# Kernel tuning notes

Hardware: AMD Instinct MI355X
Metric: run time of the kernel (lower is better)

Reference implementation:

```python
import jax, jax.numpy as jnp
import numpy as np

H = 12
D_MODEL = 768
H_D = D_MODEL // H


def setup_inputs() -> dict:
    key = jax.random.key(0)
    ks = jax.random.split(key, 11)
    B, S = 2, 2048
    scale_in = 1.0
    w_scale = 1.0 / np.sqrt(D_MODEL)
    inp = {
        "query": jax.random.normal(ks[0], (B, S, D_MODEL), dtype=jnp.float32),
        "key": jax.random.normal(ks[1], (B, S, D_MODEL), dtype=jnp.float32),
        "value": jax.random.normal(ks[2], (B, S, D_MODEL), dtype=jnp.float32),
        "wq": jax.random.normal(ks[3], (D_MODEL, D_MODEL), dtype=jnp.float32) * w_scale,
        "bq": jnp.zeros((D_MODEL,), dtype=jnp.float32),
        "wk": jax.random.normal(ks[4], (D_MODEL, D_MODEL), dtype=jnp.float32) * w_scale,
        "bk": jnp.zeros((D_MODEL,), dtype=jnp.float32),
        "wv": jax.random.normal(ks[5], (D_MODEL, D_MODEL), dtype=jnp.float32) * w_scale,
        "bv": jnp.zeros((D_MODEL,), dtype=jnp.float32),
        "wo": jax.random.normal(ks[6], (D_MODEL, D_MODEL), dtype=jnp.float32) * w_scale,
        "bo": jnp.zeros((D_MODEL,), dtype=jnp.float32),
    }
    return inp


def reference(query, key, value, wq, bq, wk, bk, wv, bv, wo, bo):
    B, S, _ = query.shape
    # QKV projections, split into heads: [B, H, S, h_d]
    def proj(x, w, b):
        y = jnp.einsum("bsd,de->bse", x, w) + b
        return y.reshape(B, S, H, H_D).transpose(0, 2, 1, 3)

    q = proj(query, wq, bq)
    k = proj(key, wk, bk)
    v = proj(value, wv, bv)

    # scaled dot-product attention (dropout disabled / eval mode)
    scores = jnp.einsum("bhsd,bhtd->bhst", q, k) / jnp.sqrt(jnp.float32(H_D))
    wm = jax.nn.softmax(scores, axis=-1)  # [B, H, S, S]
    out = jnp.einsum("bhst,bhtd->bhsd", wm, v)

    # merge heads and output projection
    out = out.transpose(0, 2, 1, 3).reshape(B, S, D_MODEL)
    out = jnp.einsum("bsd,de->bse", out, wo) + bo
    return out
```

## Files before the change

### kernel.cpp

```cpp
#include <hip/hip_runtime.h>

#define H 12
#define DM 768
#define HD 64
#define SEQ 2048
#define BATCH 2
#define MROWS (BATCH*SEQ)

typedef __attribute__((ext_vector_type(8))) short short8;
typedef __attribute__((ext_vector_type(4))) float f32x4;
typedef __attribute__((ext_vector_type(16))) float f32x16;
using u16 = unsigned short;
using u32 = unsigned int;

__device__ __forceinline__ float bf2f(u16 u) { return __uint_as_float(((u32)u) << 16); }
__device__ __forceinline__ u16 f2bf(float x) {
  u32 u = __float_as_uint(x);
  return (u16)((u + 0x7fffu + ((u >> 16) & 1u)) >> 16);
}
__device__ __forceinline__ u32 cvt_pk_bf16(float lo, float hi) {
  u32 r;
  asm("v_cvt_pk_bf16_f32 %0, %1, %2" : "=v"(r) : "v"(lo), "v"(hi));
  return r;
}
__device__ __forceinline__ void gl2lds16(const u16* __restrict__ g, u16* l) {
  __builtin_amdgcn_global_load_lds(
      (const __attribute__((address_space(1))) unsigned int*)g,
      (__attribute__((address_space(3))) unsigned int*)l,
      16, 0, 0);
}

#define C_SM 0.18033688011112042f

__global__ __launch_bounds__(256) void transpose_w4(const float* __restrict__ w0, const float* __restrict__ w1,
                                                    const float* __restrict__ w2, const float* __restrict__ w3,
                                                    u16* __restrict__ dst0)
{
  __shared__ u16 Ts[64][72];
  const float* src = blockIdx.z == 0 ? w0 : blockIdx.z == 1 ? w1 : blockIdx.z == 2 ? w2 : w3;
  u16* dst = dst0 + (size_t)blockIdx.z * DM * DM;
  const int t = threadIdx.x;
  const int r0 = blockIdx.y * 64, c0 = blockIdx.x * 64;
  const int row = t >> 2, cq = (t & 3) * 16;
  const float* sp = src + (size_t)(r0 + row) * DM + c0 + cq;
  #pragma unroll
  for (int g = 0; g < 4; ++g) {
    float4 a = *reinterpret_cast<const float4*>(sp + g * 4);
    Ts[row][cq + g * 4 + 0] = f2bf(a.x);
    Ts[row][cq + g * 4 + 1] = f2bf(a.y);
    Ts[row][cq + g * 4 + 2] = f2bf(a.z);
    Ts[row][cq + g * 4 + 3] = f2bf(a.w);
  }
  __syncthreads();
  union { uint4 v[2]; u16 e[16]; } pk;
  #pragma unroll
  for (int j = 0; j < 16; ++j) pk.e[j] = Ts[cq + j][row];
  uint4* dp = reinterpret_cast<uint4*>(dst + (size_t)(c0 + row) * DM + r0 + cq);
  dp[0] = pk.v[0];
  dp[1] = pk.v[1];
}

template<int BM, bool AF32>
__device__ __forceinline__ void gemm_core(const void* __restrict__ Av, const u16* __restrict__ Bt,
                                          const float* __restrict__ bias, void* __restrict__ dstv,
                                          int mode, int bx, int by, float outScale)
{
  constexpr int AFR = BM / 32;
  constexpr int ACH = BM / 32;
  __shared__ u16 As[BM * 64];
  __shared__ u16 Bs[128 * 64];
  const int t = threadIdx.x;
  const int lane = t & 63, w = t >> 6;
  const int l15 = lane & 15, l4 = lane >> 4;
  const int m0 = by * BM, n0 = bx * 128;
  const int wr = (w >> 1) * (BM / 2), wc = (w & 1) * 64;

  f32x4 acc[AFR][4] = {};

  for (int kt = 0; kt < DM / 64; ++kt) {
    const int k0 = kt * 64;
    #pragma unroll
    for (int c = 0; c < ACH; ++c) {
      const int id = c * 256 + t;
      const int row = id >> 3, xc = id & 7;
      const int db = row * 128 + ((xc * 16) ^ ((row & 7) << 4));
      if (AF32) {
        const float* Af = reinterpret_cast<const float*>(Av) + (size_t)(m0 + row) * DM + k0 + xc * 8;
        float4 a0 = *reinterpret_cast<const float4*>(Af);
        float4 a1 = *reinterpret_cast<const float4*>(Af + 4);
        uint4 v;
        v.x = cvt_pk_bf16(a0.x, a0.y);
        v.y = cvt_pk_bf16(a0.z, a0.w);
        v.z = cvt_pk_bf16(a1.x, a1.y);
        v.w = cvt_pk_bf16(a1.z, a1.w);
        *reinterpret_cast<uint4*>(reinterpret_cast<char*>(As) + db) = v;
      } else {
        uint4 va = *reinterpret_cast<const uint4*>(reinterpret_cast<const u16*>(Av) +
                   (size_t)(m0 + row) * DM + k0 + xc * 8);
        *reinterpret_cast<uint4*>(reinterpret_cast<char*>(As) + db) = va;
      }
    }
    #pragma unroll
    for (int c = 0; c < 4; ++c) {
      const int id = c * 256 + t;
      const int row = id >> 3, xc = id & 7;
      const int db = row * 128 + ((xc * 16) ^ ((row & 7) << 4));
      uint4 vb = *reinterpret_cast<const uint4*>(Bt + (size_t)(n0 + row) * DM + k0 + xc * 8);
      *reinterpret_cast<uint4*>(reinterpret_cast<char*>(Bs) + db) = vb;
    }
    __syncthreads();
    #pragma unroll
    for (int ks = 0; ks < 2; ++ks) {
      short8 ag[AFR], bg[4];
      #pragma unroll
      for (int i = 0; i < AFR; ++i) {
        const int ar = wr + i * 16 + l15;
        ag[i] = *reinterpret_cast<const short8*>(reinterpret_cast<const char*>(As) +
                 ar * 128 + ((ks * 64 + l4 * 16) ^ ((ar & 7) << 4)));
      }
      #pragma unroll
      for (int j = 0; j < 4; ++j) {
        const int br = wc + j * 16 + l15;
        bg[j] = *reinterpret_cast<const short8*>(reinterpret_cast<const char*>(Bs) +
                 br * 128 + ((ks * 64 + l4 * 16) ^ ((br & 7) << 4)));
      }
      #pragma unroll
      for (int i = 0; i < AFR; ++i)
        #pragma unroll
        for (int j = 0; j < 4; ++j)
          acc[i][j] = __builtin_amdgcn_mfma_f32_16x16x32_bf16(ag[i], bg[j], acc[i][j], 0, 0, 0);
    }
    __syncthreads();
  }

  #pragma unroll
  for (int j = 0; j < 4; ++j) {
    const int gcol = n0 + wc + j * 16 + l15;
    const float bb = bias[gcol];
    #pragma unroll
    for (int i = 0; i < AFR; ++i) {
      const int grow = m0 + wr + i * 16 + l4 * 4;
      if (mode == 2) {
        float* dst = reinterpret_cast<float*>(dstv);
        #pragma unroll
        for (int r = 0; r < 4; ++r)
          dst[(size_t)(grow + r) * DM + gcol] = acc[i][j][r] + bb;
      } else {
        u16* dst = reinterpret_cast<u16*>(dstv);
        const int b = grow >> 11, s = grow & (SEQ - 1);
        const int h = gcol >> 6, d = gcol & 63;
        if (mode == 0) {
          #pragma unroll
          for (int r = 0; r < 4; ++r)
            dst[((size_t)(b * H + h) * SEQ + s + r) * HD + d] = f2bf((acc[i][j][r] + bb) * outScale);
        } else {
          union { uint2 v; u16 e[4]; } pk;
          #pragma unroll
          for (int r = 0; r < 4; ++r) pk.e[r] = f2bf(acc[i][j][r] + bb);
          *reinterpret_cast<uint2*>(dst + ((size_t)(b * H + h) * HD + d) * SEQ + s) = pk.v;
        }
      }
    }
  }
}

__global__ __launch_bounds__(256) void gemm_qkv_kernel(
    const float* __restrict__ xq, const float* __restrict__ xk, const float* __restrict__ xv,
    const u16* __restrict__ wT, const float* __restrict__ bq, const float* __restrict__ bk,
    const float* __restrict__ bv, u16* __restrict__ Qb, u16* __restrict__ Kb, u16* __restrict__ Vtb)
{
  const int flat = blockIdx.z * 384 + blockIdx.y * 6 + blockIdx.x;
  const int nb = (flat & 7) * 144 + (flat >> 3);
  const int z = nb / 384, rem = nb % 384;
  const int by = rem / 6, bx = rem % 6;
  const float* A    = z == 0 ? xq : z == 1 ? xk : xv;
  const u16* Bt     = wT + (size_t)z * DM * DM;
  const float* bias = z == 0 ? bq : z == 1 ? bk : bv;
  u16* dst          = z == 0 ? Qb : z == 1 ? Kb : Vtb;
  const float sc    = z == 1 ? C_SM : 1.0f;
  gemm_core<64, true>(A, Bt, bias, dst, z == 2 ? 1 : 0, bx, by, sc);
}

__global__ __launch_bounds__(256) void gemm_o_kernel(const u16* __restrict__ A, const u16* __restrict__ woT,
                                                     const float* __restrict__ bo, float* __restrict__ out)
{
  const int flat = blockIdx.y * 6 + blockIdx.x;
  const int nb = (flat & 7) * 96 + (flat >> 3);
  gemm_core<32, false>(A, woT, bo, out, 2, nb % 6, nb / 6, 1.0f);
}

__global__ __launch_bounds__(256) void attn_kernel(const u16* __restrict__ Q, const u16* __restrict__ K,
                                                   const u16* __restrict__ Vt,
                                                   float* __restrict__ Op0, float* __restrict__ Op1,
                                                   float* __restrict__ Lp0, float* __restrict__ Lp1)
{
  __shared__ u16 Ks[2][64 * 64];
  __shared__ u16 Vs[2][64 * 64];
  const int t = threadIdx.x;
  const int lane = t & 63, w = t >> 6;
  const int l31 = lane & 31, hi = lane >> 5;
  const int flat = blockIdx.y * 32 + blockIdx.x;
  const int nbid = (flat & 7) * 96 + (flat >> 3);
  const int bh = nbid >> 5;
  const int rem = nbid & 31;
  const int q0 = (rem >> 1) * 128;
  const int half = rem & 1;
  const int kv0 = half * (SEQ / 2);
  const size_t qbase  = ((size_t)bh * SEQ + q0) * HD;
  const size_t kbase0 = (size_t)bh * SEQ * HD;
  const size_t vtbase = (size_t)bh * HD * SEQ;
  float* __restrict__ Op = half ? Op1 : Op0;
  float* __restrict__ Lp = half ? Lp1 : Lp0;

  const int r8 = lane >> 3;
  const int pcol = ((lane & 7) ^ r8) * 8;

  short8 qf[4];
  {
    const u16* qp = Q + qbase + (size_t)(w * 32 + l31) * HD + hi * 8;
    #pragma unroll
    for (int ks = 0; ks < 4; ++ks)
      qf[ks] = *reinterpret_cast<const short8*>(qp + ks * 16);
  }

  #pragma unroll
  for (int j = 0; j < 2; ++j) {
    const int ci = w * 2 + j;
    const int row = ci * 8 + r8;
    gl2lds16(K + kbase0 + (size_t)(kv0 + row) * HD + pcol, &Ks[0][ci * 512]);
    gl2lds16(Vt + vtbase + (size_t)row * SEQ + kv0 + pcol, &Vs[0][ci * 512]);
  }

  f32x16 oacc[2] = {};
  float l_s = 0.f;
  int cur = 0;

  for (int kt = 0; kt < SEQ / 2 / 64; ++kt) {
    asm volatile("s_waitcnt vmcnt(0)" ::: "memory");
    __builtin_amdgcn_s_barrier();

    if (kt + 1 < SEQ / 2 / 64) {
      const int nxt = cur ^ 1;
      #pragma unroll
      for (int j = 0; j < 2; ++j) {
        const int ci = w * 2 + j;
        const int row = ci * 8 + r8;
        gl2lds16(K + kbase0 + (size_t)(kv0 + (kt + 1) * 64 + row) * HD + pcol, &Ks[nxt][ci * 512]);
        gl2lds16(Vt + vtbase + (size_t)row * SEQ + kv0 + (kt + 1) * 64 + pcol, &Vs[nxt][ci * 512]);
      }
    }

    f32x16 s0 = {}, s1 = {};
    __builtin_amdgcn_s_setprio(1);
    #pragma unroll
    for (int ks = 0; ks < 4; ++ks) {
      const int cb = ks * 32 + hi * 16;
      short8 kf0 = *reinterpret_cast<const short8*>(reinterpret_cast<const char*>(Ks[cur]) +
                   l31 * 128 + (cb ^ ((l31 & 7) << 4)));
      short8 kf1 = *reinterpret_cast<const short8*>(reinterpret_cast<const char*>(Ks[cur]) +
                   (32 + l31) * 128 + (cb ^ ((l31 & 7) << 4)));
      s0 = __builtin_amdgcn_mfma_f32_32x32x16_bf16(kf0, qf[ks], s0, 0, 0, 0);
      s1 = __builtin_amdgcn_mfma_f32_32x32x16_bf16(kf1, qf[ks], s1, 0, 0, 0);
    }
    __builtin_amdgcn_s_setprio(0);

    float p0[16], p1[16], psum = 0.f;
    #pragma unroll
    for (int r = 0; r < 16; ++r) {
      p0[r] = exp2f(s0[r]);
      p1[r] = exp2f(s1[r]);
      psum += p0[r] + p1[r];
    }
    l_s += psum;

    __builtin_amdgcn_s_setprio(1);
    #pragma unroll
    for (int ks2 = 0; ks2 < 4; ++ks2) {
      const float* P = (ks2 < 2) ? p0 : p1;
      const int ro = (ks2 & 1) * 8;
      u32 a0 = cvt_pk_bf16(P[ro + 0], P[ro + 1]);
      u32 a1 = cvt_pk_bf16(P[ro + 2], P[ro + 3]);
      u32 b0 = cvt_pk_bf16(P[ro + 4], P[ro + 5]);
      u32 b1 = cvt_pk_bf16(P[ro + 6], P[ro + 7]);
      asm volatile("v_permlane32_swap_b32 %0, %1" : "+v"(a0), "+v"(b0));
      asm volatile("v_permlane32_swap_b32 %0, %1" : "+v"(a1), "+v"(b1));
      union { u32 u[4]; short8 s; } pa;
      pa.u[0] = a0; pa.u[1] = a1; pa.u[2] = b0; pa.u[3] = b1;
      const int cb2 = ks2 * 32 + hi * 16;
      #pragma unroll
      for (int dt = 0; dt < 2; ++dt) {
        const int vr = dt * 32 + l31;
        short8 vf = *reinterpret_cast<const short8*>(reinterpret_cast<const char*>(Vs[cur]) +
                    vr * 128 + (cb2 ^ ((vr & 7) << 4)));
        oacc[dt] = __builtin_amdgcn_mfma_f32_32x32x16_bf16(pa.s, vf, oacc[dt], 0, 0, 0);
      }
    }
    __builtin_amdgcn_s_setprio(0);
    cur ^= 1;
  }

  const float l_tot = l_s + __shfl_xor(l_s, 32);
  if (hi == 0)
    Lp[(size_t)bh * SEQ + q0 + w * 32 + l31] = l_tot;
  #pragma unroll
  for (int r = 0; r < 16; ++r) {
    const int qo = (r & 3) + 8 * (r >> 2) + 4 * hi;
    const size_t base = ((size_t)bh * SEQ + q0 + w * 32 + qo) * HD;
    Op[base + l31]      = oacc[0][r];
    Op[base + 32 + l31] = oacc[1][r];
  }
}

__global__ __launch_bounds__(256) void attn_merge(const float* __restrict__ Op0, const float* __restrict__ Op1,
                                                  const float* __restrict__ Lp0, const float* __restrict__ Lp1,
                                                  u16* __restrict__ Ab)
{
  const int id = blockIdx.x * 256 + threadIdx.x;
  const int row = id >> 4, dc = (id & 15) * 4;
  const int bh = row >> 11, q = row & (SEQ - 1);
  const int b = bh / H, h = bh % H;
  const float inv = 1.f / (Lp0[row] + Lp1[row]);
  float4 o0 = *reinterpret_cast<const float4*>(Op0 + (size_t)row * HD + dc);
  float4 o1 = *reinterpret_cast<const float4*>(Op1 + (size_t)row * HD + dc);
  uint2 o;
  o.x = cvt_pk_bf16((o0.x + o1.x) * inv, (o0.y + o1.y) * inv);
  o.y = cvt_pk_bf16((o0.z + o1.z) * inv, (o0.w + o1.w) * inv);
  *reinterpret_cast<uint2*>(Ab + ((size_t)(b * SEQ + q)) * DM + h * HD + dc) = o;
}

extern "C" void kernel_launch(void* const* d_in, const int* in_sizes, int n_in,
                              void* d_out, int out_size, void* d_ws, size_t ws_size,
                              hipStream_t stream)
{
  const float* q  = (const float*)d_in[0];
  const float* k  = (const float*)d_in[1];
  const float* v  = (const float*)d_in[2];
  const float* wq = (const float*)d_in[3];
  const float* bq = (const float*)d_in[4];
  const float* wk = (const float*)d_in[5];
  const float* bk = (const float*)d_in[6];
  const float* wv = (const float*)d_in[7];
  const float* bv = (const float*)d_in[8];
  const float* wo = (const float*)d_in[9];
  const float* bo = (const float*)d_in[10];

  u16* ws = (u16*)d_ws;
  const size_t WSZ = (size_t)DM * DM;
  const size_t TSZ = (size_t)MROWS * DM;
  const size_t NQ  = (size_t)BATCH * H * SEQ;
  u16* wT  = ws;
  u16* Qb  = ws + 4 * WSZ;
  u16* Kb  = Qb + TSZ;
  u16* Vtb = Kb + TSZ;
  u16* Ab  = Vtb + TSZ;
  float* Op0 = (float*)(Ab + TSZ);
  float* Op1 = Op0 + TSZ;
  float* Lp0 = Op1 + TSZ;
  float* Lp1 = Lp0 + NQ;

  transpose_w4<<<dim3(12, 12, 4), 256, 0, stream>>>(wq, wk, wv, wo, wT);
  gemm_qkv_kernel<<<dim3(6, 64, 3), 256, 0, stream>>>(q, k, v, wT, bq, bk, bv, Qb, Kb, Vtb);
  attn_kernel<<<dim3(32, 24), 256, 0, stream>>>(Qb, Kb, Vtb, Op0, Op1, Lp0, Lp1);
  attn_merge<<<dim3((int)(NQ * 16 / 256)), 256, 0, stream>>>(Op0, Op1, Lp0, Lp1, Ab);
  gemm_o_kernel<<<dim3(6, 128), 256, 0, stream>>>(Ab, wT + 3 * WSZ, bo, (float*)d_out);
}
```

Baseline: 117.9 us.

## Load K/V fragments directly from global memory in attention, dropping LDS staging

The attention kernel no longer stages K and V tiles through double-buffered shared memory with global_load_lds and barriers. Instead each wave loads its MFMA operand fragments straight from global memory into registers every iteration. This removes LDS traffic, barriers and the software pipeline. The cost is that four waves redundantly fetch the same K/V data through L1/L2 with no prefetch overlap, and register pressure rises.

```diff
diff --git a/kernel.cpp b/kernel.cpp
--- a/kernel.cpp
+++ b/kernel.cpp
@@ -22,12 +22,6 @@
   u32 r;
   asm("v_cvt_pk_bf16_f32 %0, %1, %2" : "=v"(r) : "v"(lo), "v"(hi));
   return r;
-}
-__device__ __forceinline__ void gl2lds16(const u16* __restrict__ g, u16* l) {
-  __builtin_amdgcn_global_load_lds(
-      (const __attribute__((address_space(1))) unsigned int*)g,
-      (__attribute__((address_space(3))) unsigned int*)l,
-      16, 0, 0);
 }
 
 #define C_SM 0.18033688011112042f
@@ -194,8 +188,6 @@
                                                    float* __restrict__ Op0, float* __restrict__ Op1,
                                                    float* __restrict__ Lp0, float* __restrict__ Lp1)
 {
-  __shared__ u16 Ks[2][64 * 64];
-  __shared__ u16 Vs[2][64 * 64];
   const int t = threadIdx.x;
   const int lane = t & 63, w = t >> 6;
   const int l31 = lane & 31, hi = lane >> 5;
@@ -212,9 +204,6 @@
   float* __restrict__ Op = half ? Op1 : Op0;
   float* __restrict__ Lp = half ? Lp1 : Lp0;
 
-  const int r8 = lane >> 3;
-  const int pcol = ((lane & 7) ^ r8) * 8;
-
   short8 qf[4];
   {
     const u16* qp = Q + qbase + (size_t)(w * 32 + l31) * HD + hi * 8;
@@ -223,46 +212,32 @@
       qf[ks] = *reinterpret_cast<const short8*>(qp + ks * 16);
   }
 
-  #pragma unroll
-  for (int j = 0; j < 2; ++j) {
-    const int ci = w * 2 + j;
-    const int row = ci * 8 + r8;
-    gl2lds16(K + kbase0 + (size_t)(kv0 + row) * HD + pcol, &Ks[0][ci * 512]);
-    gl2lds16(Vt + vtbase + (size_t)row * SEQ + kv0 + pcol, &Vs[0][ci * 512]);
-  }
+  const u16* kp = K + kbase0 + (size_t)(kv0 + l31) * HD + hi * 8;
+  const u16* vp = Vt + vtbase + (size_t)l31 * SEQ + kv0 + hi * 8;
 
   f32x16 oacc[2] = {};
   float l_s = 0.f;
-  int cur = 0;
 
   for (int kt = 0; kt < SEQ / 2 / 64; ++kt) {
-    asm volatile("s_waitcnt vmcnt(0)" ::: "memory");
-    __builtin_amdgcn_s_barrier();
-
-    if (kt + 1 < SEQ / 2 / 64) {
-      const int nxt = cur ^ 1;
-      #pragma unroll
-      for (int j = 0; j < 2; ++j) {
-        const int ci = w * 2 + j;
-        const int row = ci * 8 + r8;
-        gl2lds16(K + kbase0 + (size_t)(kv0 + (kt + 1) * 64 + row) * HD + pcol, &Ks[nxt][ci * 512]);
-        gl2lds16(Vt + vtbase + (size_t)row * SEQ + kv0 + (kt + 1) * 64 + pcol, &Vs[nxt][ci * 512]);
-      }
-    }
+    short8 kf0[4], kf1[4], vf[4][2];
+    const u16* kpt = kp + (size_t)(kt * 64) * HD;
+    #pragma unroll
+    for (int ks = 0; ks < 4; ++ks) {
+      kf0[ks] = *reinterpret_cast<const short8*>(kpt + ks * 16);
+      kf1[ks] = *reinterpret_cast<const short8*>(kpt + (size_t)32 * HD + ks * 16);
+    }
+    #pragma unroll
+    for (int ks2 = 0; ks2 < 4; ++ks2)
+      #pragma unroll
+      for (int dt = 0; dt < 2; ++dt)
+        vf[ks2][dt] = *reinterpret_cast<const short8*>(vp + (size_t)(dt * 32) * SEQ + kt * 64 + ks2 * 16);
 
     f32x16 s0 = {}, s1 = {};
-    __builtin_amdgcn_s_setprio(1);
     #pragma unroll
     for (int ks = 0; ks < 4; ++ks) {
-      const int cb = ks * 32 + hi * 16;
-      short8 kf0 = *reinterpret_cast<const short8*>(reinterpret_cast<const char*>(Ks[cur]) +
-                   l31 * 128 + (cb ^ ((l31 & 7) << 4)));
-      short8 kf1 = *reinterpret_cast<const short8*>(reinterpret_cast<const char*>(Ks[cur]) +
-                   (32 + l31) * 128 + (cb ^ ((l31 & 7) << 4)));
-      s0 = __builtin_amdgcn_mfma_f32_32x32x16_bf16(kf0, qf[ks], s0, 0, 0, 0);
-      s1 = __builtin_amdgcn_mfma_f32_32x32x16_bf16(kf1, qf[ks], s1, 0, 0, 0);
-    }
-    __builtin_amdgcn_s_setprio(0);
+      s0 = __builtin_amdgcn_mfma_f32_32x32x16_bf16(kf0[ks], qf[ks], s0, 0, 0, 0);
+      s1 = __builtin_amdgcn_mfma_f32_32x32x16_bf16(kf1[ks], qf[ks], s1, 0, 0, 0);
+    }
 
     float p0[16], p1[16], psum = 0.f;
     #pragma unroll
@@ -273,7 +248,6 @@
     }
     l_s += psum;
 
-    __builtin_amdgcn_s_setprio(1);
     #pragma unroll
     for (int ks2 = 0; ks2 < 4; ++ks2) {
       const float* P = (ks2 < 2) ? p0 : p1;
@@ -286,17 +260,10 @@
       asm volatile("v_permlane32_swap_b32 %0, %1" : "+v"(a1), "+v"(b1));
       union { u32 u[4]; short8 s; } pa;
       pa.u[0] = a0; pa.u[1] = a1; pa.u[2] = b0; pa.u[3] = b1;
-      const int cb2 = ks2 * 32 + hi * 16;
-      #pragma unroll
-      for (int dt = 0; dt < 2; ++dt) {
-        const int vr = dt * 32 + l31;
-        short8 vf = *reinterpret_cast<const short8*>(reinterpret_cast<const char*>(Vs[cur]) +
-                    vr * 128 + (cb2 ^ ((vr & 7) << 4)));
-        oacc[dt] = __builtin_amdgcn_mfma_f32_32x32x16_bf16(pa.s, vf, oacc[dt], 0, 0, 0);
-      }
-    }
-    __builtin_amdgcn_s_setprio(0);
-    cur ^= 1;
+      #pragma unroll
+      for (int dt = 0; dt < 2; ++dt)
+        oacc[dt] = __builtin_amdgcn_mfma_f32_32x32x16_bf16(pa.s, vf[ks2][dt], oacc[dt], 0, 0, 0);
+    }
   }
 
   const float l_tot = l_s + __shfl_xor(l_s, 32);
```

Result: slower. 150.2 us (+27.5%).

## Triple-buffer K/V tiles and compute softmax row sums with MFMA

Applied to the files above, without the earlier changes.

The attention loop moves from double to triple buffering of K/V tiles in shared memory, prefetching two tiles ahead and waiting only on the older loads (vmcnt(4)) instead of draining all outstanding loads each iteration. The scalar exp-sum reduction is replaced by an extra MFMA that multiplies the bf16 probability tile by a ones vector, accumulating row sums in the matrix unit. The cost is more LDS per block, one extra MFMA per k-step, and redundant wrapped prefetches past the end. The row sums now come from bf16-rounded probabilities, so they are consistent with the values used in P·V.

```diff
diff --git a/kernel.cpp b/kernel.cpp
--- a/kernel.cpp
+++ b/kernel.cpp
@@ -194,8 +194,8 @@
                                                    float* __restrict__ Op0, float* __restrict__ Op1,
                                                    float* __restrict__ Lp0, float* __restrict__ Lp1)
 {
-  __shared__ u16 Ks[2][64 * 64];
-  __shared__ u16 Vs[2][64 * 64];
+  __shared__ u16 Ks[3][64 * 64];
+  __shared__ u16 Vs[3][64 * 64];
   const int t = threadIdx.x;
   const int lane = t & 63, w = t >> 6;
   const int l31 = lane & 31, hi = lane >> 5;
@@ -211,6 +211,7 @@
   const size_t vtbase = (size_t)bh * HD * SEQ;
   float* __restrict__ Op = half ? Op1 : Op0;
   float* __restrict__ Lp = half ? Lp1 : Lp0;
+  constexpr int NT = SEQ / 2 / 64;
 
   const int r8 = lane >> 3;
   const int pcol = ((lane & 7) ^ r8) * 8;
@@ -223,31 +224,35 @@
       qf[ks] = *reinterpret_cast<const short8*>(qp + ks * 16);
   }
 
-  #pragma unroll
-  for (int j = 0; j < 2; ++j) {
-    const int ci = w * 2 + j;
-    const int row = ci * 8 + r8;
-    gl2lds16(K + kbase0 + (size_t)(kv0 + row) * HD + pcol, &Ks[0][ci * 512]);
-    gl2lds16(Vt + vtbase + (size_t)row * SEQ + kv0 + pcol, &Vs[0][ci * 512]);
-  }
+  auto STAGE = [&](int pt, int buf) {
+    #pragma unroll
+    for (int j = 0; j < 2; ++j) {
+      const int ci = w * 2 + j;
+      const int row = ci * 8 + r8;
+      gl2lds16(K + kbase0 + (size_t)(kv0 + pt * 64 + row) * HD + pcol, &Ks[buf][ci * 512]);
+      gl2lds16(Vt + vtbase + (size_t)row * SEQ + kv0 + pt * 64 + pcol, &Vs[buf][ci * 512]);
+    }
+  };
+
+  STAGE(0, 0);
+  STAGE(1, 1);
+
+  short8 ones;
+  #pragma unroll
+  for (int j = 0; j < 8; ++j) ones[j] = (short)0x3F80;
 
   f32x16 oacc[2] = {};
-  float l_s = 0.f;
+  f32x16 accL = {};
   int cur = 0;
 
-  for (int kt = 0; kt < SEQ / 2 / 64; ++kt) {
-    asm volatile("s_waitcnt vmcnt(0)" ::: "memory");
+  for (int kt = 0; kt < NT; ++kt) {
+    asm volatile("s_waitcnt vmcnt(4)" ::: "memory");
     __builtin_amdgcn_s_barrier();
 
-    if (kt + 1 < SEQ / 2 / 64) {
-      const int nxt = cur ^ 1;
-      #pragma unroll
-      for (int j = 0; j < 2; ++j) {
-        const int ci = w * 2 + j;
-        const int row = ci * 8 + r8;
-        gl2lds16(K + kbase0 + (size_t)(kv0 + (kt + 1) * 64 + row) * HD + pcol, &Ks[nxt][ci * 512]);
-        gl2lds16(Vt + vtbase + (size_t)row * SEQ + kv0 + (kt + 1) * 64 + pcol, &Vs[nxt][ci * 512]);
-      }
+    {
+      const int pt = (kt + 2) & (NT - 1);
+      const int pbuf = (cur + 2) % 3;
+      STAGE(pt, pbuf);
     }
 
     f32x16 s0 = {}, s1 = {};
@@ -264,14 +269,12 @@
     }
     __builtin_amdgcn_s_setprio(0);
 
-    float p0[16], p1[16], psum = 0.f;
+    float p0[16], p1[16];
     #pragma unroll
     for (int r = 0; r < 16; ++r) {
       p0[r] = exp2f(s0[r]);
       p1[r] = exp2f(s1[r]);
-      psum += p0[r] + p1[r];
-    }
-    l_s += psum;
+    }
 
     __builtin_amdgcn_s_setprio(1);
     #pragma unroll
@@ -286,22 +289,26 @@
       asm volatile("v_permlane32_swap_b32 %0, %1" : "+v"(a1), "+v"(b1));
       union { u32 u[4]; short8 s; } pa;
       pa.u[0] = a0; pa.u[1] = a1; pa.u[2] = b0; pa.u[3] = b1;
-      const int cb2 = ks2 * 32 + hi * 16;
+      accL = __builtin_amdgcn_mfma_f32_32x32x16_bf16(pa.s, ones, accL, 0, 0, 0);
       #pragma unroll
       for (int dt = 0; dt < 2; ++dt) {
         const int vr = dt * 32 + l31;
         short8 vf = *reinterpret_cast<const short8*>(reinterpret_cast<const char*>(Vs[cur]) +
-                    vr * 128 + (cb2 ^ ((vr & 7) << 4)));
+                    vr * 128 + ((ks2 * 32 + hi * 16) ^ ((vr & 7) << 4)));
         oacc[dt] = __builtin_amdgcn_mfma_f32_32x32x16_bf16(pa.s, vf, oacc[dt], 0, 0, 0);
       }
     }
     __builtin_amdgcn_s_setprio(0);
-    cur ^= 1;
-  }
-
-  const float l_tot = l_s + __shfl_xor(l_s, 32);
-  if (hi == 0)
-    Lp[(size_t)bh * SEQ + q0 + w * 32 + l31] = l_tot;
+    cur = (cur == 2) ? 0 : cur + 1;
+  }
+
+  if (l31 == 0) {
+    #pragma unroll
+    for (int r = 0; r < 16; ++r) {
+      const int qo = (r & 3) + 8 * (r >> 2) + 4 * hi;
+      Lp[(size_t)bh * SEQ + q0 + w * 32 + qo] = accL[r];
+    }
+  }
   #pragma unroll
   for (int r = 0; r < 16; ++r) {
     const int qo = (r & 3) + 8 * (r >> 2) + 4 * hi;
```

Result: faster. 108.2 us (-8.2%).
